# Kernel optimization log

Measured on AMD Instinct MI355X. Metric: run time of the kernel, lower is better.

Reference implementation:

```python
import jax, jax.numpy as jnp
import numpy as np

EPS = 1e-5

def adain_norm(x):
    # per-(batch,channel) instance normalization over spatial dims (AdaIN projection)
    mean = jnp.mean(x, axis=(2, 3), keepdims=True)
    var = jnp.var(x, axis=(2, 3), keepdims=True)
    return (x - mean) / jnp.sqrt(var + EPS)

def conv1x1(x, w, b):
    # x: [B,C,H,W], w: [O,C], b: [O]
    return jnp.einsum('bchw,oc->bohw', x, w) + b[None, :, None, None]

def setup_inputs() -> dict:
    key = jax.random.key(0)
    ks = jax.random.split(key, 10)
    B, C, H, W = 4, 512, 64, 64
    s = 1.0 / np.sqrt(C)
    return {
        'x': jax.random.normal(ks[0], (B, C, H, W), jnp.float32),
        'y': jax.random.normal(ks[1], (B, C, H, W), jnp.float32),
        'f_w': jax.random.normal(ks[2], (C, C), jnp.float32) * s,
        'f_b': jnp.zeros((C,), jnp.float32),
        'g_w': jax.random.normal(ks[3], (C, C), jnp.float32) * s,
        'g_b': jnp.zeros((C,), jnp.float32),
        'h_w': jax.random.normal(ks[4], (C, C), jnp.float32) * s,
        'h_b': jnp.zeros((C,), jnp.float32),
        'out_w': jax.random.normal(ks[5], (C, C), jnp.float32) * s,
        'out_b': jnp.zeros((C,), jnp.float32),
    }

def reference(x, y, f_w, f_b, g_w, g_b, h_w, h_b, out_w, out_b):
    B, C, H, W = x.shape
    HW = H * W
    xn = adain_norm(x)
    yn = adain_norm(y)
    # 1x1 conv projections, flattened over spatial dims
    f = conv1x1(xn, f_w, f_b).reshape(B, C, HW)   # [B,C,HWx]
    g = conv1x1(yn, g_w, g_b).reshape(B, C, HW)   # [B,C,HWy]
    energy = jnp.einsum('bci,bcj->bij', f, g)     # [B,HWx,HWy]
    correlation = jax.nn.softmax(energy, axis=-1)
    h = conv1x1(y, h_w, h_b).reshape(B, C, HW)    # [B,C,HWy]
    # residual = h @ correlation^T -> [B,C,HWx]
    residual = jnp.einsum('bcj,bij->bci', h, correlation).reshape(B, C, H, W)
    residual = conv1x1(residual, out_w, out_b)
    return x + residual
```

## Files before the change

kernel.cpp:

```cpp
#include <hip/hip_runtime.h>
#include <stdint.h>

#define HW 4096
#define NC 512
#define NB 4

typedef __attribute__((ext_vector_type(8))) _Float16 f16x8;
typedef __attribute__((ext_vector_type(4))) float f32x4;
typedef __attribute__((ext_vector_type(4))) unsigned short ush4;
typedef __attribute__((ext_vector_type(8))) unsigned short ush8;

typedef __attribute__((address_space(1))) const void* as1_cvp;
typedef __attribute__((address_space(3))) void* as3_vp;

__device__ __forceinline__ unsigned short f2h(float f) {
  union { _Float16 h; unsigned short u; } c;
  c.h = (_Float16)f;
  return c.u;
}
__device__ __forceinline__ float h2f(unsigned short u) {
  union { unsigned short u; _Float16 h; } c;
  c.u = u;
  return (float)c.h;
}

__global__ __launch_bounds__(256) void moments_k(const float* __restrict__ x,
                                                 const float* __restrict__ y,
                                                 float* __restrict__ stats) {
  int bid = blockIdx.x;
  int tens = bid >> 11;
  int row = bid & 2047;
  const float* src = (tens ? y : x) + (size_t)row * HW;
  float s = 0.f, s2 = 0.f;
  for (int j = threadIdx.x; j < HW / 4; j += 256) {
    float4 v = ((const float4*)src)[j];
    s += (v.x + v.y) + (v.z + v.w);
    s2 += (v.x * v.x + v.y * v.y) + (v.z * v.z + v.w * v.w);
  }
  #pragma unroll
  for (int o = 32; o; o >>= 1) { s += __shfl_down(s, o); s2 += __shfl_down(s2, o); }
  __shared__ float rs[8];
  int w = threadIdx.x >> 6;
  if ((threadIdx.x & 63) == 0) { rs[w] = s; rs[4 + w] = s2; }
  __syncthreads();
  if (threadIdx.x == 0) {
    float S = (rs[0] + rs[1]) + (rs[2] + rs[3]);
    float S2 = (rs[4] + rs[5]) + (rs[6] + rs[7]);
    float mean = S * (1.f / HW);
    float var = S2 * (1.f / HW) - mean * mean;
    stats[tens * 4096 + row] = mean;
    stats[tens * 4096 + 2048 + row] = rsqrtf(var + 1e-5f);
  }
}

__global__ __launch_bounds__(256) void transnorm_k(const float* __restrict__ x,
                                                   const float* __restrict__ y,
                                                   const float* __restrict__ stats,
                                                   unsigned short* __restrict__ xnT,
                                                   unsigned short* __restrict__ ynT,
                                                   unsigned short* __restrict__ yH) {
  __shared__ float tile[64][65];
  __shared__ float ms[64], rsd[64];
  int zi = blockIdx.z;
  int b = zi >> 1, mode = zi & 1;
  int i0 = blockIdx.x * 64, c0 = blockIdx.y * 64;
  const float* src = mode ? y : x;
  int t = threadIdx.x;
  int c = t >> 2;
  int isub = (t & 3) << 4;
  if (t < 64) {
    int srow = (mode ? 4096 : 0) + b * NC + c0 + t;
    ms[t] = stats[srow];
    rsd[t] = stats[srow + 2048];
  }
  const float4* sp = (const float4*)(src + ((size_t)(b * NC + c0 + c)) * HW + i0 + isub);
  #pragma unroll
  for (int k = 0; k < 4; ++k) {
    float4 v = sp[k];
    int ib = isub + k * 4;
    tile[ib + 0][c] = v.x;
    tile[ib + 1][c] = v.y;
    tile[ib + 2][c] = v.z;
    tile[ib + 3][c] = v.w;
    if (mode) {
      ush4 yo;
      yo[0] = f2h(v.x); yo[1] = f2h(v.y); yo[2] = f2h(v.z); yo[3] = f2h(v.w);
      *(ush4*)(yH + ((size_t)(b * NC + c0 + c)) * HW + i0 + isub + k * 4) = yo;
    }
  }
  __syncthreads();
  int i = t >> 2;
  int cc = (t & 3) << 4;
  size_t obase = ((size_t)b * HW + i0 + i) * NC + c0 + cc;
  unsigned short* dst = mode ? ynT : xnT;
  #pragma unroll
  for (int h = 0; h < 2; ++h) {
    ush8 o;
    #pragma unroll
    for (int e = 0; e < 8; ++e) {
      int ce = cc + h * 8 + e;
      o[e] = f2h((tile[i][ce] - ms[ce]) * rsd[ce]);
    }
    *(ush8*)(dst + obase + h * 8) = o;
  }
}

__global__ __launch_bounds__(256) void castw_k(const float* __restrict__ fw,
                                               const float* __restrict__ gw,
                                               const float* __restrict__ hw_,
                                               const float* __restrict__ ow,
                                               unsigned short* __restrict__ fwT,
                                               unsigned short* __restrict__ gwT,
                                               unsigned short* __restrict__ hwT,
                                               unsigned short* __restrict__ owB) {
  __shared__ float tile[64][65];
  int which = blockIdx.z;
  const float* src = which == 0 ? fw : which == 1 ? gw : which == 2 ? hw_ : ow;
  unsigned short* dst = which == 0 ? fwT : which == 1 ? gwT : which == 2 ? hwT : owB;
  int r0 = blockIdx.x * 64, c0 = blockIdx.y * 64;
  int t = threadIdx.x;
  int r = t >> 2;
  int csub = (t & 3) << 4;
  const float4* sp = (const float4*)(src + (size_t)(r0 + r) * 512 + c0 + csub);
  if (which == 3) {
    #pragma unroll
    for (int k = 0; k < 4; ++k) {
      float4 v = sp[k];
      ush4 o;
      o[0] = f2h(v.x); o[1] = f2h(v.y); o[2] = f2h(v.z); o[3] = f2h(v.w);
      *(ush4*)(dst + (size_t)(r0 + r) * 512 + c0 + csub + k * 4) = o;
    }
    return;
  }
  #pragma unroll
  for (int k = 0; k < 4; ++k) {
    float4 v = sp[k];
    int cb = csub + k * 4;
    tile[cb + 0][r] = v.x;
    tile[cb + 1][r] = v.y;
    tile[cb + 2][r] = v.z;
    tile[cb + 3][r] = v.w;
  }
  __syncthreads();
  int cw = t >> 2;
  int rsub = (t & 3) << 4;
  #pragma unroll
  for (int h = 0; h < 2; ++h) {
    ush8 o;
    #pragma unroll
    for (int e = 0; e < 8; ++e) o[e] = f2h(tile[cw][rsub + h * 8 + e]);
    *(ush8*)(dst + (size_t)(c0 + cw) * 512 + r0 + rsub + h * 8) = o;
  }
}

__global__ __launch_bounds__(256) void repl_k(const unsigned short* __restrict__ W2,
                                              unsigned short* __restrict__ W2x2) {
  int idx = blockIdx.x * 256 + threadIdx.x;
  int o = idx >> 7;
  int k = (idx & 127) * 8;
  ush8 v = *(const ush8*)(W2 + (size_t)o * 512 + (k & 511));
  *(ush8*)(W2x2 + (size_t)o * 1024 + k) = v;
}

__global__ __launch_bounds__(256) void dotrows_h(const unsigned short* __restrict__ A,
                                                 const float* __restrict__ vec,
                                                 float* __restrict__ out) {
  int row = blockIdx.x * 4 + (threadIdx.x >> 6);
  int lane = threadIdx.x & 63;
  ush8 a = *(const ush8*)(A + (size_t)row * 512 + lane * 8);
  float s = 0.f;
  #pragma unroll
  for (int e = 0; e < 8; ++e) s += h2f(a[e]) * vec[lane * 8 + e];
  #pragma unroll
  for (int o = 32; o; o >>= 1) s += __shfl_down(s, o);
  if (lane == 0) out[row] = s;
}

__global__ __launch_bounds__(256) void b2_k(const float* __restrict__ Wf,
                                            const float* __restrict__ hb,
                                            const float* __restrict__ ob,
                                            float* __restrict__ out) {
  int row = blockIdx.x * 4 + (threadIdx.x >> 6);
  int lane = threadIdx.x & 63;
  const float4* a = (const float4*)(Wf + (size_t)row * 512) + lane * 2;
  float4 x0 = a[0], x1 = a[1];
  const float4* hv = (const float4*)hb + lane * 2;
  float4 h0 = hv[0], h1 = hv[1];
  float s = x0.x * h0.x + x0.y * h0.y + x0.z * h0.z + x0.w * h0.w
          + x1.x * h1.x + x1.y * h1.y + x1.z * h1.z + x1.w * h1.w;
  #pragma unroll
  for (int o = 32; o; o >>= 1) s += __shfl_down(s, o);
  if (lane == 0) out[row] = ob[row] + s;
}

__global__ __launch_bounds__(256) void softmax_h(unsigned short* __restrict__ S) {
  unsigned short* row = S + (size_t)blockIdx.x * HW;
  int t = threadIdx.x;
  ush8 a0 = *(const ush8*)(row + t * 16);
  ush8 a1 = *(const ush8*)(row + t * 16 + 8);
  float v[16];
  #pragma unroll
  for (int e = 0; e < 8; ++e) { v[e] = h2f(a0[e]); v[8 + e] = h2f(a1[e]); }
  float mx = -3.0e38f;
  #pragma unroll
  for (int e = 0; e < 16; ++e) mx = fmaxf(mx, v[e]);
  #pragma unroll
  for (int o = 32; o; o >>= 1) mx = fmaxf(mx, __shfl_down(mx, o));
  __shared__ float red[8];
  int w = t >> 6;
  if ((t & 63) == 0) red[w] = mx;
  __syncthreads();
  mx = fmaxf(fmaxf(red[0], red[1]), fmaxf(red[2], red[3]));
  float sum = 0.f;
  #pragma unroll
  for (int e = 0; e < 16; ++e) { v[e] = __expf(v[e] - mx); sum += v[e]; }
  #pragma unroll
  for (int o = 32; o; o >>= 1) sum += __shfl_down(sum, o);
  if ((t & 63) == 0) red[4 + w] = sum;
  __syncthreads();
  float inv = 1.f / ((red[4] + red[5]) + (red[6] + red[7]));
  ush8 o0, o1;
  #pragma unroll
  for (int e = 0; e < 8; ++e) { o0[e] = f2h(v[e] * inv); o1[e] = f2h(v[8 + e] * inv); }
  *(ush8*)(row + t * 16) = o0;
  *(ush8*)(row + t * 16 + 8) = o1;
}

__global__ __launch_bounds__(256, 2) void gemm_ntp(
    const unsigned short* __restrict__ A, long long sA, int lda,
    const unsigned short* __restrict__ Bm, long long sB, int ldb,
    void* __restrict__ Cp, long long sC, long long sCs, int ldc,
    int K, int out_f32, int ls,
    const float* __restrict__ bias_m, const float* __restrict__ bias_n,
    const float* __restrict__ add_src, long long sAdd,
    const unsigned short* __restrict__ B2, const float* __restrict__ bias_n2,
    int zsw) {
  __shared__ short lsA[2][128 * 64];
  __shared__ short lsB[2][128 * 64];
  const int t = threadIdx.x;
  const int lane = t & 63;
  const int w = t >> 6;
  const int wm = w >> 1, wn = w & 1;
  const long long bz = blockIdx.z;
  if ((int)bz >= zsw) { Bm = B2; bias_n = bias_n2; }
  const long long bg = bz >> ls;
  const int sp = (int)(bz - (bg << ls));
  const long long koff = (long long)sp * K;
  const unsigned short* Ab = A + bz * sA * (ls ? 0 : 1) + (ls ? bg * sA : 0) + koff
                           + (size_t)blockIdx.x * 128 * lda;
  const unsigned short* Bb = Bm + bg * sB + koff + (size_t)blockIdx.y * 128 * ldb;

  f32x4 zero = {0.f, 0.f, 0.f, 0.f};
  f32x4 acc[4][4];
  #pragma unroll
  for (int i = 0; i < 4; ++i)
    #pragma unroll
    for (int j = 0; j < 4; ++j) acc[i][j] = zero;

  const int nkt = K >> 6;

  auto STAGE = [&](int buf, int kt) {
    const int kbase = kt << 6;
    #pragma unroll
    for (int i = 0; i < 4; ++i) {
      int q = t + i * 256;
      int r = q >> 3, xx = q & 7;
      int gk = kbase + ((xx ^ (r & 7)) << 3);
      __builtin_amdgcn_global_load_lds((as1_cvp)(const void*)(Ab + (size_t)r * lda + gk),
                                       (as3_vp)(void*)(&lsA[buf][q << 3]), 16, 0, 0);
      __builtin_amdgcn_global_load_lds((as1_cvp)(const void*)(Bb + (size_t)r * ldb + gk),
                                       (as3_vp)(void*)(&lsB[buf][q << 3]), 16, 0, 0);
    }
  };

  STAGE(0, 0);
  __syncthreads();
  int cur = 0;
  for (int kt = 0; kt < nkt; ++kt) {
    if (kt + 1 < nkt) STAGE(cur ^ 1, kt + 1);
    #pragma unroll
    for (int ks = 0; ks < 2; ++ks) {
      f16x8 av[4], bv[4];
      const int xl = ks * 4 + (lane >> 4);
      const int rr = lane & 15;
      #pragma unroll
      for (int mb = 0; mb < 4; ++mb) {
        int row = wm * 64 + mb * 16 + rr;
        av[mb] = *(const f16x8*)&lsA[cur][(row << 6) + ((xl ^ (row & 7)) << 3)];
      }
      #pragma unroll
      for (int nb = 0; nb < 4; ++nb) {
        int row = wn * 64 + nb * 16 + rr;
        bv[nb] = *(const f16x8*)&lsB[cur][(row << 6) + ((xl ^ (row & 7)) << 3)];
      }
      __builtin_amdgcn_s_setprio(1);
      #pragma unroll
      for (int mb = 0; mb < 4; ++mb)
        #pragma unroll
        for (int nb = 0; nb < 4; ++nb)
          acc[mb][nb] = __builtin_amdgcn_mfma_f32_16x16x32_f16(av[mb], bv[nb], acc[mb][nb], 0, 0, 0);
      __builtin_amdgcn_s_setprio(0);
    }
    __syncthreads();
    cur ^= 1;
  }

  const int mb0 = blockIdx.x * 128 + wm * 64;
  const int nb0 = blockIdx.y * 128 + wn * 64;
  const int cn = lane & 15;
  const int rq = (lane >> 4) << 2;
  float* cf = (float*)Cp;
  unsigned short* ch = (unsigned short*)Cp;
  #pragma unroll
  for (int mb = 0; mb < 4; ++mb) {
    #pragma unroll
    for (int nb = 0; nb < 4; ++nb) {
      int n = nb0 + nb * 16 + cn;
      float bn = bias_n ? bias_n[n] : 0.f;
      #pragma unroll
      for (int r = 0; r < 4; ++r) {
        int m = mb0 + mb * 16 + rq + r;
        float vv = acc[mb][nb][r] + bn;
        if (bias_m) vv += bias_m[m];
        if (add_src) vv += add_src[bg * sAdd + (size_t)m * ldc + n];
        size_t off = (size_t)(bg * sC) + (size_t)sp * sCs + (size_t)m * ldc + n;
        if (out_f32) cf[off] = vv;
        else ch[off] = f2h(vv);
      }
    }
  }
}

__global__ __launch_bounds__(512, 2) void gemm_nt2(
    const unsigned short* __restrict__ A, long long sA, int lda,
    const unsigned short* __restrict__ Bm, long long sB, int ldb,
    void* __restrict__ Cp, long long sC, int ldc,
    int K, int out_f32,
    const float* __restrict__ bias_n, long long sBn) {
  __shared__ short lsA[2][256 * 64];
  __shared__ short lsB[2][256 * 64];
  const int t = threadIdx.x;
  const int lane = t & 63;
  const int w = t >> 6;
  const int wm = w >> 2, wn = w & 3;
  const long long bz = blockIdx.z;
  const unsigned short* Ab = A + bz * sA + (size_t)blockIdx.x * 256 * lda;
  const unsigned short* Bb = Bm + bz * sB + (size_t)blockIdx.y * 256 * ldb;

  f32x4 zero = {0.f, 0.f, 0.f, 0.f};
  f32x4 acc[8][4];
  #pragma unroll
  for (int i = 0; i < 8; ++i)
    #pragma unroll
    for (int j = 0; j < 4; ++j) acc[i][j] = zero;

  const int rr = lane & 15;
  const int xl = lane >> 4;
  const int nkt = K >> 6;

  auto STAGE = [&](int buf, int kt) {
    const int kbase = kt << 6;
    #pragma unroll
    for (int i = 0; i < 4; ++i) {
      int q = t + i * 512;
      int r = q >> 3, xx = q & 7;
      int gk = kbase + ((xx ^ (r & 7)) << 3);
      __builtin_amdgcn_global_load_lds((as1_cvp)(const void*)(Ab + (size_t)r * lda + gk),
                                       (as3_vp)(void*)(&lsA[buf][q << 3]), 16, 0, 0);
      __builtin_amdgcn_global_load_lds((as1_cvp)(const void*)(Bb + (size_t)r * ldb + gk),
                                       (as3_vp)(void*)(&lsB[buf][q << 3]), 16, 0, 0);
    }
  };

  STAGE(0, 0);
  __syncthreads();
  int cur = 0;
  for (int kt = 0; kt < nkt; ++kt) {
    if (kt + 1 < nkt) STAGE(cur ^ 1, kt + 1);
    #pragma unroll
    for (int ks = 0; ks < 2; ++ks) {
      f16x8 av[8], bv[4];
      const int cb = ks * 4 + xl;
      #pragma unroll
      for (int mb = 0; mb < 8; ++mb) {
        int row = wm * 128 + mb * 16 + rr;
        av[mb] = *(const f16x8*)&lsA[cur][(row << 6) + ((cb ^ (row & 7)) << 3)];
      }
      #pragma unroll
      for (int nb = 0; nb < 4; ++nb) {
        int row = wn * 64 + nb * 16 + rr;
        bv[nb] = *(const f16x8*)&lsB[cur][(row << 6) + ((cb ^ (row & 7)) << 3)];
      }
      __builtin_amdgcn_s_setprio(1);
      #pragma unroll
      for (int mb = 0; mb < 8; ++mb)
        #pragma unroll
        for (int nb = 0; nb < 4; ++nb)
          acc[mb][nb] = __builtin_amdgcn_mfma_f32_16x16x32_f16(av[mb], bv[nb], acc[mb][nb], 0, 0, 0);
      __builtin_amdgcn_s_setprio(0);
    }
    __syncthreads();
    cur ^= 1;
  }

  const int mb0 = blockIdx.x * 256 + wm * 128;
  const int nb0 = blockIdx.y * 256 + wn * 64;
  const int cn = lane & 15;
  const int rq = (lane >> 4) << 2;
  float* cf = (float*)Cp;
  unsigned short* ch = (unsigned short*)Cp;
  #pragma unroll
  for (int mb = 0; mb < 8; ++mb) {
    #pragma unroll
    for (int nb = 0; nb < 4; ++nb) {
      int n = nb0 + nb * 16 + cn;
      float bn = bias_n ? bias_n[bz * sBn + n] : 0.f;
      #pragma unroll
      for (int r = 0; r < 4; ++r) {
        int m = mb0 + mb * 16 + rq + r;
        float vv = acc[mb][nb][r] + bn;
        size_t off = (size_t)(bz * sC) + (size_t)m * ldc + n;
        if (out_f32) cf[off] = vv;
        else ch[off] = f2h(vv);
      }
    }
  }
}

extern "C" void kernel_launch(void* const* d_in, const int* in_sizes, int n_in,
                              void* d_out, int out_size, void* d_ws, size_t ws_size,
                              hipStream_t stream) {
  const float* x = (const float*)d_in[0];
  const float* y = (const float*)d_in[1];
  const float* f_w = (const float*)d_in[2];
  const float* f_b = (const float*)d_in[3];
  const float* g_w = (const float*)d_in[4];
  const float* g_b = (const float*)d_in[5];
  const float* h_w = (const float*)d_in[6];
  const float* h_b = (const float*)d_in[7];
  const float* out_w = (const float*)d_in[8];
  const float* out_b = (const float*)d_in[9];
  float* out = (float*)d_out;
  (void)g_b;

  char* ws = (char*)d_ws;
  size_t off = 0;
  auto alloc = [&](size_t bytes) -> char* {
    char* p = ws + off;
    off += (bytes + 255) & ~(size_t)255;
    return p;
  };
  const size_t TN = (size_t)NB * HW * NC;
  const size_t WN = (size_t)512 * 512;
  float* stats = (float*)alloc(8192 * sizeof(float));
  unsigned short* fwT = (unsigned short*)alloc(WN * 2);
  unsigned short* gwT = (unsigned short*)alloc(WN * 2);
  unsigned short* hwT = (unsigned short*)alloc(WN * 2);
  unsigned short* owB = (unsigned short*)alloc(WN * 2);
  unsigned short* W1T = (unsigned short*)alloc(WN * 2);
  unsigned short* W2 = (unsigned short*)alloc(WN * 2);
  unsigned short* W2x2 = (unsigned short*)alloc((size_t)512 * 1024 * 2);
  float* vv = (float*)alloc(512 * 4);
  float* b2 = (float*)alloc(512 * 4);
  float* wj = (float*)alloc((size_t)NB * HW * 4);
  unsigned short* xnT = (unsigned short*)alloc(TN * 2);
  unsigned short* ynT = (unsigned short*)alloc(TN * 2);
  unsigned short* yH = (unsigned short*)alloc(TN * 2);
  unsigned short* fB = (unsigned short*)alloc(TN * 2);
  unsigned short* Zp = (unsigned short*)alloc((size_t)NB * HW * 1024 * 2);
  size_t remain = ws_size > off ? ws_size - off : 0;
  const size_t SB = (size_t)HW * HW * 2;
  int G, R = HW;
  if (remain >= 4 * SB)      { G = 4; }
  else if (remain >= 2 * SB) { G = 2; }
  else if (remain >= SB)     { G = 1; }
  else {
    G = 1;
    while (R > 128 && (size_t)R * HW * 2 > remain) R >>= 1;
  }
  unsigned short* Sh = (unsigned short*)alloc((size_t)G * R * HW * 2);
  if (off > ws_size) return;

  const long long PS = (long long)HW * NC;
  const int BIG = 1 << 30;

  castw_k<<<dim3(8, 8, 4), dim3(256), 0, stream>>>(f_w, g_w, h_w, out_w,
                                                   fwT, gwT, hwT, owB);
  moments_k<<<dim3(4096), dim3(256), 0, stream>>>(x, y, stats);
  transnorm_k<<<dim3(64, 8, 8), dim3(256), 0, stream>>>(x, y, stats, xnT, ynT, yH);

  dotrows_h<<<dim3(128), dim3(256), 0, stream>>>(gwT, f_b, vv);
  b2_k<<<dim3(128), dim3(256), 0, stream>>>(out_w, h_b, out_b, b2);
  gemm_ntp<<<dim3(4, 4, 1), dim3(256), 0, stream>>>(
      gwT, 0, 512, fwT, 0, 512, W1T, 0, 0, 512, 512, 0, 0,
      nullptr, nullptr, nullptr, 0, nullptr, nullptr, BIG);
  gemm_ntp<<<dim3(4, 4, 1), dim3(256), 0, stream>>>(
      owB, 0, 512, hwT, 0, 512, W2, 0, 0, 512, 512, 0, 0,
      nullptr, nullptr, nullptr, 0, nullptr, nullptr, BIG);
  repl_k<<<dim3(256), dim3(256), 0, stream>>>(W2, W2x2);
  dotrows_h<<<dim3(NB * HW / 4), dim3(256), 0, stream>>>(ynT, vv, wj);
  gemm_ntp<<<dim3(32, 4, NB), dim3(256), 0, stream>>>(
      xnT, PS, NC, W1T, 0, NC, fB, PS, 0, NC, NC, 0, 0,
      nullptr, nullptr, nullptr, 0, nullptr, nullptr, BIG);

  for (int b0 = 0; b0 < NB; b0 += G) {
    for (int r0 = 0; r0 < HW; r0 += R) {
      if (R >= 256) {
        gemm_nt2<<<dim3(R / 256, HW / 256, G), dim3(512), 0, stream>>>(
            fB + ((size_t)b0 * HW + r0) * NC, PS, NC,
            ynT + (size_t)b0 * PS, PS, NC,
            Sh, (long long)R * HW, HW, NC, 0,
            wj + (size_t)b0 * HW, HW);
      } else {
        gemm_ntp<<<dim3(R / 128, 32, G), dim3(256), 0, stream>>>(
            fB + ((size_t)b0 * HW + r0) * NC, PS, NC,
            ynT + (size_t)b0 * PS, PS, NC,
            Sh, (long long)R * HW, 0, HW, NC, 0, 0,
            nullptr, wj + (size_t)b0 * HW, nullptr, 0, nullptr, nullptr, BIG);
      }
      softmax_h<<<dim3(G * R), dim3(256), 0, stream>>>(Sh);
      gemm_ntp<<<dim3(R / 128, 4, G * 2), dim3(256), 0, stream>>>(
          Sh, (long long)R * HW, HW,
          yH + (size_t)b0 * NC * HW, (long long)NC * HW, HW,
          Zp + ((size_t)b0 * HW + r0) * 1024, (long long)R * 1024, 512, 1024,
          HW / 2, 0, 1,
          nullptr, nullptr, nullptr, 0, nullptr, nullptr, BIG);
    }
  }
  gemm_ntp<<<dim3(4, 32, NB), dim3(256), 0, stream>>>(
      W2x2, 0, 1024, Zp, (long long)HW * 1024, 1024,
      out, (long long)NC * HW, 0, HW, 1024, 1, 0,
      b2, nullptr, x, (long long)NC * HW, nullptr, nullptr, BIG);
}
```

Measured before the change: 391.0 us.

## Replace GEMM kernels with triple-buffered 256x128 tile kernel using waitcnt-based pipelining

```diff
diff --git a/kernel.cpp b/kernel.cpp
--- a/kernel.cpp
+++ b/kernel.cpp
@@ -331,34 +331,38 @@
   }
 }
 
-__global__ __launch_bounds__(512, 2) void gemm_nt2(
+__global__ __launch_bounds__(512, 1) void gemm_ntr(
     const unsigned short* __restrict__ A, long long sA, int lda,
     const unsigned short* __restrict__ Bm, long long sB, int ldb,
-    void* __restrict__ Cp, long long sC, int ldc,
-    int K, int out_f32,
-    const float* __restrict__ bias_n, long long sBn) {
-  __shared__ short lsA[2][256 * 64];
-  __shared__ short lsB[2][256 * 64];
+    void* __restrict__ Cp, long long sC, long long sCs, int ldc,
+    int K, int out_f32, int ls,
+    const float* __restrict__ bias_m,
+    const float* __restrict__ bias_n, long long sBn,
+    const float* __restrict__ add_src, long long sAdd) {
+  __shared__ short lsA[3][256 * 64];
+  __shared__ short lsB[3][128 * 64];
   const int t = threadIdx.x;
   const int lane = t & 63;
   const int w = t >> 6;
-  const int wm = w >> 2, wn = w & 3;
+  const int wm = w >> 1, wn = w & 1;
   const long long bz = blockIdx.z;
-  const unsigned short* Ab = A + bz * sA + (size_t)blockIdx.x * 256 * lda;
-  const unsigned short* Bb = Bm + bz * sB + (size_t)blockIdx.y * 256 * ldb;
+  const long long bg = bz >> ls;
+  const int sp = (int)(bz - (bg << ls));
+  const long long koff = (long long)sp * K;
+  const unsigned short* Ab = A + bg * sA + koff + (size_t)blockIdx.x * 256 * lda;
+  const unsigned short* Bb = Bm + bg * sB + koff + (size_t)blockIdx.y * 128 * ldb;
 
   f32x4 zero = {0.f, 0.f, 0.f, 0.f};
-  f32x4 acc[8][4];
-  #pragma unroll
-  for (int i = 0; i < 8; ++i)
+  f32x4 acc[4][4];
+  #pragma unroll
+  for (int i = 0; i < 4; ++i)
     #pragma unroll
     for (int j = 0; j < 4; ++j) acc[i][j] = zero;
 
-  const int rr = lane & 15;
-  const int xl = lane >> 4;
   const int nkt = K >> 6;
 
-  auto STAGE = [&](int buf, int kt) {
+  auto STAGE = [&](int kt) {
+    const int slot = kt % 3;
     const int kbase = kt << 6;
     #pragma unroll
     for (int i = 0; i < 4; ++i) {
@@ -366,60 +370,83 @@
       int r = q >> 3, xx = q & 7;
       int gk = kbase + ((xx ^ (r & 7)) << 3);
       __builtin_amdgcn_global_load_lds((as1_cvp)(const void*)(Ab + (size_t)r * lda + gk),
-                                       (as3_vp)(void*)(&lsA[buf][q << 3]), 16, 0, 0);
+                                       (as3_vp)(void*)(&lsA[slot][q << 3]), 16, 0, 0);
+    }
+    #pragma unroll
+    for (int i = 0; i < 2; ++i) {
+      int q = t + i * 512;
+      int r = q >> 3, xx = q & 7;
+      int gk = kbase + ((xx ^ (r & 7)) << 3);
       __builtin_amdgcn_global_load_lds((as1_cvp)(const void*)(Bb + (size_t)r * ldb + gk),
-                                       (as3_vp)(void*)(&lsB[buf][q << 3]), 16, 0, 0);
+                                       (as3_vp)(void*)(&lsB[slot][q << 3]), 16, 0, 0);
     }
   };
 
-  STAGE(0, 0);
-  __syncthreads();
-  int cur = 0;
-  for (int kt = 0; kt < nkt; ++kt) {
-    if (kt + 1 < nkt) STAGE(cur ^ 1, kt + 1);
+  auto COMPUTE = [&](int kt) {
+    const int slot = kt % 3;
     #pragma unroll
     for (int ks = 0; ks < 2; ++ks) {
-      f16x8 av[8], bv[4];
-      const int cb = ks * 4 + xl;
-      #pragma unroll
-      for (int mb = 0; mb < 8; ++mb) {
-        int row = wm * 128 + mb * 16 + rr;
-        av[mb] = *(const f16x8*)&lsA[cur][(row << 6) + ((cb ^ (row & 7)) << 3)];
+      f16x8 av[4], bv[4];
+      const int xl = ks * 4 + (lane >> 4);
+      const int rr = lane & 15;
+      #pragma unroll
+      for (int mb = 0; mb < 4; ++mb) {
+        int row = wm * 64 + mb * 16 + rr;
+        av[mb] = *(const f16x8*)&lsA[slot][(row << 6) + ((xl ^ (row & 7)) << 3)];
       }
       #pragma unroll
       for (int nb = 0; nb < 4; ++nb) {
         int row = wn * 64 + nb * 16 + rr;
-        bv[nb] = *(const f16x8*)&lsB[cur][(row << 6) + ((cb ^ (row & 7)) << 3)];
+        bv[nb] = *(const f16x8*)&lsB[slot][(row << 6) + ((xl ^ (row & 7)) << 3)];
       }
       __builtin_amdgcn_s_setprio(1);
       #pragma unroll
-      for (int mb = 0; mb < 8; ++mb)
+      for (int mb = 0; mb < 4; ++mb)
         #pragma unroll
         for (int nb = 0; nb < 4; ++nb)
           acc[mb][nb] = __builtin_amdgcn_mfma_f32_16x16x32_f16(av[mb], bv[nb], acc[mb][nb], 0, 0, 0);
       __builtin_amdgcn_s_setprio(0);
     }
-    __syncthreads();
-    cur ^= 1;
-  }
-
-  const int mb0 = blockIdx.x * 256 + wm * 128;
-  const int nb0 = blockIdx.y * 256 + wn * 64;
+  };
+
+  STAGE(0);
+  if (nkt > 1) {
+    STAGE(1);
+    asm volatile("s_waitcnt vmcnt(6)" ::: "memory");
+  } else {
+    asm volatile("s_waitcnt vmcnt(0)" ::: "memory");
+  }
+  __builtin_amdgcn_s_barrier();
+
+  for (int kt = 0; kt < nkt; ++kt) {
+    if (kt + 2 < nkt) STAGE(kt + 2);
+    COMPUTE(kt);
+    if (kt + 1 < nkt) {
+      if (kt + 2 < nkt) asm volatile("s_waitcnt vmcnt(6)" ::: "memory");
+      else              asm volatile("s_waitcnt vmcnt(0)" ::: "memory");
+      __builtin_amdgcn_s_barrier();
+    }
+  }
+
+  const int mb0 = blockIdx.x * 256 + wm * 64;
+  const int nb0 = blockIdx.y * 128 + wn * 64;
   const int cn = lane & 15;
   const int rq = (lane >> 4) << 2;
   float* cf = (float*)Cp;
   unsigned short* ch = (unsigned short*)Cp;
   #pragma unroll
-  for (int mb = 0; mb < 8; ++mb) {
+  for (int mb = 0; mb < 4; ++mb) {
     #pragma unroll
     for (int nb = 0; nb < 4; ++nb) {
       int n = nb0 + nb * 16 + cn;
-      float bn = bias_n ? bias_n[bz * sBn + n] : 0.f;
+      float bn = bias_n ? bias_n[bg * sBn + n] : 0.f;
       #pragma unroll
       for (int r = 0; r < 4; ++r) {
         int m = mb0 + mb * 16 + rq + r;
         float vv = acc[mb][nb][r] + bn;
-        size_t off = (size_t)(bz * sC) + (size_t)m * ldc + n;
+        if (bias_m) vv += bias_m[m];
+        if (add_src) vv += add_src[bg * sAdd + (size_t)m * ldc + n];
+        size_t off = (size_t)(bg * sC) + (size_t)sp * sCs + (size_t)m * ldc + n;
         if (out_f32) cf[off] = vv;
         else ch[off] = f2h(vv);
       }
@@ -499,36 +526,43 @@
       nullptr, nullptr, nullptr, 0, nullptr, nullptr, BIG);
   repl_k<<<dim3(256), dim3(256), 0, stream>>>(W2, W2x2);
   dotrows_h<<<dim3(NB * HW / 4), dim3(256), 0, stream>>>(ynT, vv, wj);
-  gemm_ntp<<<dim3(32, 4, NB), dim3(256), 0, stream>>>(
+  gemm_ntr<<<dim3(16, 4, NB), dim3(512), 0, stream>>>(
       xnT, PS, NC, W1T, 0, NC, fB, PS, 0, NC, NC, 0, 0,
-      nullptr, nullptr, nullptr, 0, nullptr, nullptr, BIG);
+      nullptr, nullptr, 0, nullptr, 0);
 
   for (int b0 = 0; b0 < NB; b0 += G) {
     for (int r0 = 0; r0 < HW; r0 += R) {
       if (R >= 256) {
-        gemm_nt2<<<dim3(R / 256, HW / 256, G), dim3(512), 0, stream>>>(
+        gemm_ntr<<<dim3(R / 256, HW / 128, G), dim3(512), 0, stream>>>(
             fB + ((size_t)b0 * HW + r0) * NC, PS, NC,
             ynT + (size_t)b0 * PS, PS, NC,
-            Sh, (long long)R * HW, HW, NC, 0,
-            wj + (size_t)b0 * HW, HW);
+            Sh, (long long)R * HW, 0, HW, NC, 0, 0,
+            nullptr, wj + (size_t)b0 * HW, HW, nullptr, 0);
+        softmax_h<<<dim3(G * R), dim3(256), 0, stream>>>(Sh);
+        gemm_ntr<<<dim3(R / 256, NC / 128, G * 2), dim3(512), 0, stream>>>(
+            Sh, (long long)R * HW, HW,
+            yH + (size_t)b0 * NC * HW, (long long)NC * HW, HW,
+            Zp + ((size_t)b0 * HW + r0) * 1024, (long long)R * 1024, 512, 1024,
+            HW / 2, 0, 1,
+            nullptr, nullptr, 0, nullptr, 0);
       } else {
         gemm_ntp<<<dim3(R / 128, 32, G), dim3(256), 0, stream>>>(
             fB + ((size_t)b0 * HW + r0) * NC, PS, NC,
             ynT + (size_t)b0 * PS, PS, NC,
             Sh, (long long)R * HW, 0, HW, NC, 0, 0,
             nullptr, wj + (size_t)b0 * HW, nullptr, 0, nullptr, nullptr, BIG);
-      }
-      softmax_h<<<dim3(G * R), dim3(256), 0, stream>>>(Sh);
-      gemm_ntp<<<dim3(R / 128, 4, G * 2), dim3(256), 0, stream>>>(
-          Sh, (long long)R * HW, HW,
-          yH + (size_t)b0 * NC * HW, (long long)NC * HW, HW,
-          Zp + ((size_t)b0 * HW + r0) * 1024, (long long)R * 1024, 512, 1024,
-          HW / 2, 0, 1,
-          nullptr, nullptr, nullptr, 0, nullptr, nullptr, BIG);
-    }
-  }
-  gemm_ntp<<<dim3(4, 32, NB), dim3(256), 0, stream>>>(
+        softmax_h<<<dim3(G * R), dim3(256), 0, stream>>>(Sh);
+        gemm_ntp<<<dim3(R / 128, 4, G * 2), dim3(256), 0, stream>>>(
+            Sh, (long long)R * HW, HW,
+            yH + (size_t)b0 * NC * HW, (long long)NC * HW, HW,
+            Zp + ((size_t)b0 * HW + r0) * 1024, (long long)R * 1024, 512, 1024,
+            HW / 2, 0, 1,
+            nullptr, nullptr, nullptr, 0, nullptr, nullptr, BIG);
+      }
+    }
+  }
+  gemm_ntr<<<dim3(2, 32, NB), dim3(512), 0, stream>>>(
       W2x2, 0, 1024, Zp, (long long)HW * 1024, 1024,
       out, (long long)NC * HW, 0, HW, 1024, 1, 0,
-      b2, nullptr, x, (long long)NC * HW, nullptr, nullptr, BIG);
-}
+      b2, nullptr, 0, x, (long long)NC * HW);
+}
```

Measured after the change: 446.6 us. 14.2% more time.
